# Optimization experiments

Measured on AMD Instinct MI355X. Metric: run time of the kernel, lower is better.

The kernel has to match this reference:

```python
import jax, jax.numpy as jnp
import numpy as np

D_MODEL, N_HEADS, D_K, BASE, EPS = 1024, 16, 64, 10000, 1e-6
SCALE = 1.0 / np.sqrt(D_K)


def rope(x):
    # x: [b, s, h, d]
    b, s, h, d = x.shape
    d2 = d // 2
    theta = 1.0 / (BASE ** (jnp.arange(0, d, 2, dtype=jnp.float32) / d))  # [d2]
    idx_theta = jnp.arange(s, dtype=jnp.float32)[:, None] * theta[None, :]  # [s, d2]
    idx_theta2 = jnp.concatenate([idx_theta, idx_theta], axis=1)  # [s, d]
    cos = jnp.cos(idx_theta2)[None, :, None, :]
    sin = jnp.sin(idx_theta2)[None, :, None, :]
    neg_half = jnp.concatenate([-x[..., d2:], x[..., :d2]], axis=-1)
    return x * cos + neg_half * sin


def setup_inputs() -> dict:
    key = jax.random.key(0)
    ks = jax.random.split(key, 10)
    B, S = 2, 2048
    std = 1.0 / np.sqrt(D_MODEL)
    return {
        "h": jax.random.normal(ks[0], (B, S, D_MODEL), dtype=jnp.float32),
        "wq": jax.random.normal(ks[1], (D_MODEL, N_HEADS * D_K), dtype=jnp.float32) * std,
        "bq": jnp.zeros((N_HEADS * D_K,), dtype=jnp.float32),
        "wk": jax.random.normal(ks[2], (D_MODEL, N_HEADS * D_K), dtype=jnp.float32) * std,
        "bk": jnp.zeros((N_HEADS * D_K,), dtype=jnp.float32),
        "wv": jax.random.normal(ks[3], (D_MODEL, N_HEADS * D_K), dtype=jnp.float32) * std,
        "bv": jnp.zeros((N_HEADS * D_K,), dtype=jnp.float32),
        "wo": jax.random.normal(ks[4], (N_HEADS * D_K, D_MODEL), dtype=jnp.float32) * std,
        "bo": jnp.zeros((D_MODEL,), dtype=jnp.float32),
        "g": jnp.ones((D_MODEL,), dtype=jnp.float32),
    }


def reference(h, wq, bq, wk, bk, wv, bv, wo, bo, g):
    B, S, _ = h.shape
    h_res = h
    # RMSNorm
    hn = h * jax.lax.rsqrt(jnp.mean(h * h, axis=-1, keepdims=True) + EPS) * g
    mh = (B, S, N_HEADS, D_K)
    q = (hn @ wq + bq).reshape(mh)
    k = (hn @ wk + bk).reshape(mh)
    v = (hn @ wv + bv).reshape(mh)
    q, k = rope(q), rope(k)
    attn = jnp.einsum('bihd,bjhd->bhij', q, k) * SCALE
    mask = jnp.tril(jnp.ones((S, S), dtype=bool))
    attn = jnp.where(mask, attn, -jnp.inf)
    attn = jax.nn.softmax(attn, axis=-1)
    out = jnp.einsum('bhij,bjhd->bihd', attn, v).reshape(B, S, N_HEADS * D_K)
    return out @ wo + bo + h_res
```

## Files before the change

### kernel.cpp

```cpp
#include <hip/hip_runtime.h>
#include <hip/hip_bf16.h>

#define D_MODEL 1024
#define NH 16
#define DK 64
#define SEQ 2048
#define BATCH 2
#define NTOK (BATCH * SEQ)
#define EPS 1e-6f

typedef __attribute__((ext_vector_type(4))) float f32x4;
typedef __attribute__((ext_vector_type(16))) float f32x16;
typedef __attribute__((ext_vector_type(8))) short s16x8;
typedef unsigned int u32;
typedef __hip_bfloat16 bf16;

#define AS1 __attribute__((address_space(1)))
#define AS3 __attribute__((address_space(3)))

static __device__ __forceinline__ s16x8 ld8(const bf16* p) {
    return *reinterpret_cast<const s16x8*>(p);
}
static __device__ __forceinline__ float b2f(short s) {
    return __uint_as_float(((u32)(unsigned short)s) << 16);
}

static __device__ __forceinline__ u32 cvtpk(float lo, float hi) {
    u32 r;
    asm volatile("v_cvt_pk_bf16_f32 %0, %1, %2" : "=v"(r) : "v"(lo), "v"(hi));
    return r;
}
static __device__ __forceinline__ void swap32(u32& a, u32& b) {
    asm volatile("v_permlane32_swap_b32 %0, %1" : "+v"(a), "+v"(b));
}
static __device__ __forceinline__ float exp2f_fast(float x) {
    float r;
    asm("v_exp_f32 %0, %1" : "=v"(r) : "v"(x));
    return r;
}
static __device__ __forceinline__ void gld_lds16(const bf16* g, bf16* l) {
    __builtin_amdgcn_global_load_lds((const AS1 void*)g, (AS3 void*)l, 16, 0, 0);
}

union W4 { s16x8 v; u32 w[4]; };

#define LDSW(arr, row, kc) ld8(&arr[(row)][(((kc) ^ ((row) & 7)) << 3)])

__global__ __launch_bounds__(256) void k_prep(const float* __restrict__ h,
                                              const float* __restrict__ g,
                                              const float* __restrict__ wq,
                                              const float* __restrict__ wk,
                                              const float* __restrict__ wv,
                                              const float* __restrict__ wo,
                                              bf16* __restrict__ hn,
                                              bf16* __restrict__ wallT,
                                              float2* __restrict__ tab) {
    const int bid = blockIdx.x;
    const int tid = threadIdx.x;
    if (bid < 4096) {
        const int row = bid;
        const float4 x = reinterpret_cast<const float4*>(h + (size_t)row * D_MODEL)[tid];
        float ss = x.x * x.x + x.y * x.y + x.z * x.z + x.w * x.w;
#pragma unroll
        for (int off = 32; off; off >>= 1) ss += __shfl_xor(ss, off);
        __shared__ float red[4];
        if ((tid & 63) == 0) red[tid >> 6] = ss;
        __syncthreads();
        const float tot = red[0] + red[1] + red[2] + red[3];
        const float rs = rsqrtf(tot * (1.0f / D_MODEL) + EPS);
        const float4 gg = reinterpret_cast<const float4*>(g)[tid];
        bf16* o = hn + (size_t)row * D_MODEL + tid * 4;
        o[0] = __float2bfloat16(x.x * rs * gg.x);
        o[1] = __float2bfloat16(x.y * rs * gg.y);
        o[2] = __float2bfloat16(x.z * rs * gg.z);
        o[3] = __float2bfloat16(x.w * rs * gg.w);
        if (row < 256) {
            const int idx = row * 256 + tid;
            const int s = idx >> 5, i = idx & 31;
            const float theta = __expf(-(float)i * 0.28782313662425572f);
            float sn, cs;
            sincosf((float)s * theta, &sn, &cs);
            tab[idx] = make_float2(cs, sn);
        }
    } else {
        __shared__ float t[32][33];
        const int bid2 = bid - 4096;
        const int kt = (bid2 & 31) * 32;
        const int by = bid2 >> 5;
        const int nt = by * 32;
        const float* W = (by < 32) ? wq : (by < 64) ? wk : (by < 96) ? wv : wo;
        const int nl = nt & (D_MODEL - 1);
        const int tx = tid & 31, ty = tid >> 5;
#pragma unroll
        for (int i = 0; i < 4; i++)
            t[ty + 8 * i][tx] = W[(size_t)(kt + ty + 8 * i) * D_MODEL + nl + tx];
        __syncthreads();
#pragma unroll
        for (int i = 0; i < 4; i++)
            wallT[(size_t)(nt + ty + 8 * i) * D_MODEL + kt + tx] = __float2bfloat16(t[tx][ty + 8 * i]);
    }
}

__global__ __launch_bounds__(256) void k_gemm64_qkv(const bf16* __restrict__ A,
                                                    const bf16* __restrict__ Bt,
                                                    const float* __restrict__ bq,
                                                    const float* __restrict__ bk,
                                                    const float* __restrict__ bv,
                                                    const float2* __restrict__ tab,
                                                    bf16* __restrict__ qb,
                                                    bf16* __restrict__ kpk,
                                                    bf16* __restrict__ vpk) {
    __shared__ __align__(16) char smem[16384];
    bf16(*As)[64] = (bf16(*)[64])smem;
    bf16(*Bs)[64] = (bf16(*)[64])(smem + 8192);
    const int tid = threadIdx.x;
    const int w = tid >> 6, lane = tid & 63, l16 = lane & 15, lq = lane >> 4;
    const int wr = w >> 1, wc = w & 1;
    const int col0 = blockIdx.x * 64;
    const int row0 = blockIdx.y * 64;
    const int grow = lane >> 3;
    const int scol = (((lane & 7) ^ grow) << 3);
    f32x4 acc[2][2];
#pragma unroll
    for (int i = 0; i < 2; i++)
#pragma unroll
        for (int j = 0; j < 2; j++) acc[i][j] = f32x4{0, 0, 0, 0};

    for (int kt = 0; kt < D_MODEL; kt += 64) {
        gld_lds16(A + (size_t)(row0 + w * 16 + grow) * D_MODEL + kt + scol,      &As[w * 16][0]);
        gld_lds16(A + (size_t)(row0 + w * 16 + 8 + grow) * D_MODEL + kt + scol,  &As[w * 16 + 8][0]);
        gld_lds16(Bt + (size_t)(col0 + w * 16 + grow) * D_MODEL + kt + scol,     &Bs[w * 16][0]);
        gld_lds16(Bt + (size_t)(col0 + w * 16 + 8 + grow) * D_MODEL + kt + scol, &Bs[w * 16 + 8][0]);
        __syncthreads();
        s16x8 af[2][2], bfr[2][2];
#pragma unroll
        for (int mi = 0; mi < 2; mi++)
#pragma unroll
            for (int ks = 0; ks < 2; ks++)
                af[mi][ks] = LDSW(As, wr * 32 + mi * 16 + l16, ks * 4 + lq);
#pragma unroll
        for (int ni = 0; ni < 2; ni++)
#pragma unroll
            for (int ks = 0; ks < 2; ks++)
                bfr[ni][ks] = LDSW(Bs, wc * 32 + ni * 16 + l16, ks * 4 + lq);
        __builtin_amdgcn_s_setprio(1);
#pragma unroll
        for (int ks = 0; ks < 2; ks++)
#pragma unroll
            for (int mi = 0; mi < 2; mi++)
#pragma unroll
                for (int ni = 0; ni < 2; ni++)
                    acc[mi][ni] = __builtin_amdgcn_mfma_f32_16x16x32_bf16(af[mi][ks], bfr[ni][ks], acc[mi][ni], 0, 0, 0);
        __builtin_amdgcn_s_setprio(0);
        __syncthreads();
    }

    const int sect = col0 >> 10;
    const int b_ = row0 >> 11;
    const int head = (col0 & 1023) >> 6;
    if (sect == 2) {
        const int e0 = (lq & 1) * 4;
        const int tileL = (row0 & (SEQ - 1)) >> 6;
        bf16* dstH = vpk + ((size_t)(b_ * NH + head) << 17);
#pragma unroll
        for (int ni = 0; ni < 2; ni++) {
            const int dloc = wc * 32 + ni * 16 + l16;
            const float bs = bv[(col0 & 1023) + dloc];
#pragma unroll
            for (int mi = 0; mi < 2; mi++) {
                const int m = wr * 2 + mi;
                size_t off = ((((size_t)(tileL * 2 + (dloc >> 5)) * 4 + m) * 64
                               + ((lq >> 1) & 1) * 32 + (dloc & 31)) << 3) + e0;
                uint2 pv;
                pv.x = cvtpk(acc[mi][ni][0] + bs, acc[mi][ni][1] + bs);
                pv.y = cvtpk(acc[mi][ni][2] + bs, acc[mi][ni][3] + bs);
                *reinterpret_cast<uint2*>(dstH + off) = pv;
            }
        }
        return;
    }
    bf16(*Cs)[72] = (bf16(*)[72])smem;
    const float* bias = (sect == 0) ? bq : bk;
#pragma unroll
    for (int ni = 0; ni < 2; ni++) {
        const int cl = wc * 32 + ni * 16 + l16;
        const float bs = bias[(col0 & 1023) + cl];
#pragma unroll
        for (int mi = 0; mi < 2; mi++) {
            const int rl = wr * 32 + mi * 16 + lq * 4;
#pragma unroll
            for (int r = 0; r < 4; r++)
                Cs[rl + r][cl] = __float2bfloat16(acc[mi][ni][r] + bs);
        }
    }
    __syncthreads();
    const int row = tid >> 2, q = tid & 3;
    const int s_ = (row0 + row) & (SEQ - 1);
    const float2* tb = tab + s_ * 32 + q * 8;
    const float qs = (sect == 0) ? 0.18033688011112042f : 1.0f;
    const s16x8 vlo = ld8(&Cs[row][q * 8]);
    const s16x8 vhi = ld8(&Cs[row][q * 8 + 32]);
    u32 plo[4], phi[4];
#pragma unroll
    for (int e2 = 0; e2 < 4; e2++) {
        float a[2], b[2];
#pragma unroll
        for (int k = 0; k < 2; k++) {
            const int e = e2 * 2 + k;
            const float2 cs = tb[e];
            const float x1 = b2f(vlo[e]), x2 = b2f(vhi[e]);
            a[k] = (x1 * cs.x - x2 * cs.y) * qs;
            b[k] = (x2 * cs.x + x1 * cs.y) * qs;
        }
        plo[e2] = cvtpk(a[0], a[1]);
        phi[e2] = cvtpk(b[0], b[1]);
    }
    if (sect == 0) {
        bf16* qdst = qb + (((size_t)(b_ * NH + head) * SEQ + s_) << 6);
        *reinterpret_cast<uint4*>(qdst + q * 8)      = make_uint4(plo[0], plo[1], plo[2], plo[3]);
        *reinterpret_cast<uint4*>(qdst + 32 + q * 8) = make_uint4(phi[0], phi[1], phi[2], phi[3]);
    } else {
        bf16* kdst = kpk + ((size_t)(b_ * NH + head) << 17);
        const int jb = s_ >> 5, j31 = s_ & 31;
        const size_t offL = (((size_t)(jb * 4 + (q >> 1)) * 64 + (q & 1) * 32 + j31) << 3);
        const size_t offH = (((size_t)(jb * 4 + ((q + 4) >> 1)) * 64 + ((q + 4) & 1) * 32 + j31) << 3);
        *reinterpret_cast<uint4*>(kdst + offL) = make_uint4(plo[0], plo[1], plo[2], plo[3]);
        *reinterpret_cast<uint4*>(kdst + offH) = make_uint4(phi[0], phi[1], phi[2], phi[3]);
    }
}

__global__ __launch_bounds__(256) void k_attn9(const bf16* __restrict__ qg,
                                               const bf16* __restrict__ kp,
                                               const bf16* __restrict__ vp,
                                               bf16* __restrict__ ao) {
    const int tid = threadIdx.x;
    const int w = tid >> 6;
    const int lane = tid & 63;
    const int l31 = lane & 31;
    const int hi = lane >> 5;
    const int bid = blockIdx.x;
    const int blk = (bid >> 3) & 15;
    const int bh  = (bid & 7) + ((bid >> 7) << 3);
    int pos;
    switch (w) {
        case 0:  pos = blk;      break;
        case 1:  pos = 31 - blk; break;
        case 2:  pos = 32 + blk; break;
        default: pos = 63 - blk; break;
    }
    const int qw = pos << 5;
    const int qrow = qw + l31;

    const bf16* qptr = qg + (((size_t)bh * SEQ + qrow) << 6) + 8 * hi;
    s16x8 qf[4];
#pragma unroll
    for (int t = 0; t < 4; t++) qf[t] = ld8(qptr + 16 * t);

    f32x16 o0, o1;
#pragma unroll
    for (int r = 0; r < 16; r++) { o0[r] = 0.0f; o1[r] = 0.0f; }
    float l4[4] = {0.0f, 0.0f, 0.0f, 0.0f};

    const int nfull = qw >> 6;
    const int ntot  = (qw + 95) >> 6;
    const bf16* kbase = kp + ((size_t)bh << 17);
    const bf16* vbase = vp + ((size_t)bh << 17);

    s16x8 kA[8], kB[8], vC[8];
#pragma unroll
    for (int t = 0; t < 8; t++) kA[t] = ld8(kbase + (((size_t)t * 64 + lane) << 3));

    auto att_step = [&](s16x8(&KC)[8], s16x8(&KN)[8], const int kt) {
        const int kb = kt << 6;
#pragma unroll
        for (int t = 0; t < 8; t++)
            vC[t] = ld8(vbase + (((size_t)(kt * 8 + t) * 64 + lane) << 3));
        f32x16 s0, s1;
#pragma unroll
        for (int r = 0; r < 16; r++) { s0[r] = 0.0f; s1[r] = 0.0f; }
        __builtin_amdgcn_s_setprio(1);
#pragma unroll
        for (int t = 0; t < 4; t++) {
            s0 = __builtin_amdgcn_mfma_f32_32x32x16_bf16(KC[t],     qf[t], s0, 0, 0, 0);
            s1 = __builtin_amdgcn_mfma_f32_32x32x16_bf16(KC[4 + t], qf[t], s1, 0, 0, 0);
        }
        __builtin_amdgcn_s_setprio(0);
        const int ktn = (kt + 1 < ntot) ? kt + 1 : kt;
#pragma unroll
        for (int t = 0; t < 8; t++)
            KN[t] = ld8(kbase + (((size_t)(ktn * 8 + t) * 64 + lane) << 3));
        float p[32];
#pragma unroll
        for (int r = 0; r < 16; r++) { p[r] = s0[r]; p[16 + r] = s1[r]; }
        if (kt >= nfull) {
#pragma unroll
            for (int r = 0; r < 32; r++) {
                const int j = kb + 8 * (r >> 2) + (r & 3) + 4 * hi;
                if (j > qrow) p[r] = -3.0e38f;
            }
        }
#pragma unroll
        for (int r = 0; r < 32; r++) { p[r] = exp2f_fast(p[r]); l4[r & 3] += p[r]; }
        u32 pk_[16];
#pragma unroll
        for (int a = 0; a < 8; a++) {
            pk_[2 * a]     = cvtpk(p[4 * a],     p[4 * a + 1]);
            pk_[2 * a + 1] = cvtpk(p[4 * a + 2], p[4 * a + 3]);
        }
        __builtin_amdgcn_s_setprio(1);
#pragma unroll
        for (int m = 0; m < 4; m++) {
            u32 b0 = pk_[4 * m],     b2 = pk_[4 * m + 2];
            u32 b1 = pk_[4 * m + 1], b3 = pk_[4 * m + 3];
            swap32(b0, b2);
            swap32(b1, b3);
            W4 B; B.w[0] = b0; B.w[1] = b1; B.w[2] = b2; B.w[3] = b3;
            o0 = __builtin_amdgcn_mfma_f32_32x32x16_bf16(vC[m],     B.v, o0, 0, 0, 0);
            o1 = __builtin_amdgcn_mfma_f32_32x32x16_bf16(vC[4 + m], B.v, o1, 0, 0, 0);
        }
        __builtin_amdgcn_s_setprio(0);
    };

    int kt = 0;
    for (;;) {
        att_step(kA, kB, kt); if (++kt == ntot) break;
        att_step(kB, kA, kt); if (++kt == ntot) break;
    }

    float rs = (l4[0] + l4[1]) + (l4[2] + l4[3]);
    rs += __shfl_xor(rs, 32);
    const float inv = 1.0f / rs;
    const int b_ = bh >> 4, h_ = bh & (NH - 1);
    bf16* orow = ao + (((size_t)(b_ * SEQ + qrow)) << 10) + (h_ << 6);
#pragma unroll
    for (int g = 0; g < 4; g++) {
        {
            uint2 val;
            val.x = cvtpk(o0[4 * g] * inv, o0[4 * g + 1] * inv);
            val.y = cvtpk(o0[4 * g + 2] * inv, o0[4 * g + 3] * inv);
            *reinterpret_cast<uint2*>(orow + 8 * g + 4 * hi) = val;
        }
        {
            uint2 val;
            val.x = cvtpk(o1[4 * g] * inv, o1[4 * g + 1] * inv);
            val.y = cvtpk(o1[4 * g + 2] * inv, o1[4 * g + 3] * inv);
            *reinterpret_cast<uint2*>(orow + 32 + 8 * g + 4 * hi) = val;
        }
    }
}

__global__ __launch_bounds__(256) void k_gemm64_out(const bf16* __restrict__ A,
                                                    const bf16* __restrict__ Bt,
                                                    const float* __restrict__ bo,
                                                    const float* __restrict__ hres,
                                                    float* __restrict__ out) {
    __shared__ __align__(16) char smem[16384];
    bf16(*As)[64] = (bf16(*)[64])smem;
    bf16(*Bs)[64] = (bf16(*)[64])(smem + 8192);
    const int tid = threadIdx.x;
    const int w = tid >> 6, lane = tid & 63, l16 = lane & 15, lq = lane >> 4;
    const int wr = w >> 1, wc = w & 1;
    const int col0 = blockIdx.x * 64;
    const int row0 = blockIdx.y * 64;
    const int grow = lane >> 3;
    const int scol = (((lane & 7) ^ grow) << 3);
    f32x4 acc[2][2];
#pragma unroll
    for (int i = 0; i < 2; i++)
#pragma unroll
        for (int j = 0; j < 2; j++) acc[i][j] = f32x4{0, 0, 0, 0};

    for (int kt = 0; kt < D_MODEL; kt += 64) {
        gld_lds16(A + (size_t)(row0 + w * 16 + grow) * D_MODEL + kt + scol,      &As[w * 16][0]);
        gld_lds16(A + (size_t)(row0 + w * 16 + 8 + grow) * D_MODEL + kt + scol,  &As[w * 16 + 8][0]);
        gld_lds16(Bt + (size_t)(col0 + w * 16 + grow) * D_MODEL + kt + scol,     &Bs[w * 16][0]);
        gld_lds16(Bt + (size_t)(col0 + w * 16 + 8 + grow) * D_MODEL + kt + scol, &Bs[w * 16 + 8][0]);
        __syncthreads();
        s16x8 af[2][2], bfr[2][2];
#pragma unroll
        for (int mi = 0; mi < 2; mi++)
#pragma unroll
            for (int ks = 0; ks < 2; ks++)
                af[mi][ks] = LDSW(As, wr * 32 + mi * 16 + l16, ks * 4 + lq);
#pragma unroll
        for (int ni = 0; ni < 2; ni++)
#pragma unroll
            for (int ks = 0; ks < 2; ks++)
                bfr[ni][ks] = LDSW(Bs, wc * 32 + ni * 16 + l16, ks * 4 + lq);
        __builtin_amdgcn_s_setprio(1);
#pragma unroll
        for (int ks = 0; ks < 2; ks++)
#pragma unroll
            for (int mi = 0; mi < 2; mi++)
#pragma unroll
                for (int ni = 0; ni < 2; ni++)
                    acc[mi][ni] = __builtin_amdgcn_mfma_f32_16x16x32_bf16(af[mi][ks], bfr[ni][ks], acc[mi][ni], 0, 0, 0);
        __builtin_amdgcn_s_setprio(0);
        __syncthreads();
    }
#pragma unroll
    for (int ni = 0; ni < 2; ni++) {
        const int col = col0 + wc * 32 + ni * 16 + l16;
        const float bs = bo[col];
#pragma unroll
        for (int mi = 0; mi < 2; mi++) {
#pragma unroll
            for (int r = 0; r < 4; r++) {
                const int row = row0 + wr * 32 + mi * 16 + lq * 4 + r;
                out[(size_t)row * D_MODEL + col] =
                    acc[mi][ni][r] + bs + hres[(size_t)row * D_MODEL + col];
            }
        }
    }
}

extern "C" void kernel_launch(void* const* d_in, const int* in_sizes, int n_in,
                              void* d_out, int out_size, void* d_ws, size_t ws_size,
                              hipStream_t stream) {
    (void)in_sizes; (void)n_in; (void)out_size; (void)ws_size;
    const float* h  = (const float*)d_in[0];
    const float* wq = (const float*)d_in[1];
    const float* bq = (const float*)d_in[2];
    const float* wk = (const float*)d_in[3];
    const float* bk = (const float*)d_in[4];
    const float* wv = (const float*)d_in[5];
    const float* bv = (const float*)d_in[6];
    const float* wo = (const float*)d_in[7];
    const float* bo = (const float*)d_in[8];
    const float* g  = (const float*)d_in[9];
    float* out = (float*)d_out;

    char* ws = (char*)d_ws;
    size_t off = 0;
    auto carve = [&](size_t bytes) {
        void* p = ws + off;
        off += (bytes + 255) & ~(size_t)255;
        return p;
    };
    bf16* hn    = (bf16*)carve((size_t)NTOK * D_MODEL * 2);
    bf16* wallT = (bf16*)carve((size_t)4 * D_MODEL * D_MODEL * 2);
    bf16* wqkvT = wallT;
    bf16* woT   = wallT + (size_t)3 * D_MODEL * D_MODEL;
    bf16* qb    = (bf16*)carve((size_t)BATCH * NH * SEQ * DK * 2);
    bf16* kpk   = (bf16*)carve((size_t)BATCH * NH * SEQ * DK * 2);
    bf16* vpk   = (bf16*)carve((size_t)BATCH * NH * SEQ * DK * 2);
    bf16* ao    = (bf16*)carve((size_t)NTOK * D_MODEL * 2);
    float2* tab = (float2*)carve((size_t)SEQ * 32 * sizeof(float2));

    k_prep<<<8192, 256, 0, stream>>>(h, g, wq, wk, wv, wo, hn, wallT, tab);
    k_gemm64_qkv<<<dim3(48, 64), 256, 0, stream>>>(hn, wqkvT, bq, bk, bv, tab, qb, kpk, vpk);
    k_attn9<<<512, 256, 0, stream>>>(qb, kpk, vpk, ao);
    k_gemm64_out<<<dim3(16, 64), 256, 0, stream>>>(ao, woT, bo, h, out);
}
```

Before: 107.2 us.

## Compute Q, K and V for one head per block to reuse A tiles

The QKV projection kernel now assigns one head per block and computes all three Q/K/V sections, loading the activation tile once and reusing it against three weight tiles. The grid shrinks threefold and each block does three times the MFMA work per barrier. The RoPE epilogue loops over Q and K through shared memory. This trades fewer blocks, higher register use and larger LDS for reduced activation traffic.

```diff
diff --git a/kernel.cpp b/kernel.cpp
--- a/kernel.cpp
+++ b/kernel.cpp
@@ -101,131 +101,142 @@
     }
 }
 
-__global__ __launch_bounds__(256) void k_gemm64_qkv(const bf16* __restrict__ A,
-                                                    const bf16* __restrict__ Bt,
-                                                    const float* __restrict__ bq,
-                                                    const float* __restrict__ bk,
-                                                    const float* __restrict__ bv,
-                                                    const float2* __restrict__ tab,
-                                                    bf16* __restrict__ qb,
-                                                    bf16* __restrict__ kpk,
-                                                    bf16* __restrict__ vpk) {
-    __shared__ __align__(16) char smem[16384];
+__global__ __launch_bounds__(256) void k_gemm64_qkv3(const bf16* __restrict__ A,
+                                                     const bf16* __restrict__ Bt,
+                                                     const float* __restrict__ bq,
+                                                     const float* __restrict__ bk,
+                                                     const float* __restrict__ bv,
+                                                     const float2* __restrict__ tab,
+                                                     bf16* __restrict__ qb,
+                                                     bf16* __restrict__ kpk,
+                                                     bf16* __restrict__ vpk) {
+    __shared__ __align__(16) char smem[32768];
     bf16(*As)[64] = (bf16(*)[64])smem;
     bf16(*Bs)[64] = (bf16(*)[64])(smem + 8192);
     const int tid = threadIdx.x;
     const int w = tid >> 6, lane = tid & 63, l16 = lane & 15, lq = lane >> 4;
     const int wr = w >> 1, wc = w & 1;
-    const int col0 = blockIdx.x * 64;
+    const int head = blockIdx.x;
     const int row0 = blockIdx.y * 64;
     const int grow = lane >> 3;
     const int scol = (((lane & 7) ^ grow) << 3);
-    f32x4 acc[2][2];
-#pragma unroll
-    for (int i = 0; i < 2; i++)
-#pragma unroll
-        for (int j = 0; j < 2; j++) acc[i][j] = f32x4{0, 0, 0, 0};
+    f32x4 acc[3][2][2];
+#pragma unroll
+    for (int s = 0; s < 3; s++)
+#pragma unroll
+        for (int i = 0; i < 2; i++)
+#pragma unroll
+            for (int j = 0; j < 2; j++) acc[s][i][j] = f32x4{0, 0, 0, 0};
 
     for (int kt = 0; kt < D_MODEL; kt += 64) {
-        gld_lds16(A + (size_t)(row0 + w * 16 + grow) * D_MODEL + kt + scol,      &As[w * 16][0]);
-        gld_lds16(A + (size_t)(row0 + w * 16 + 8 + grow) * D_MODEL + kt + scol,  &As[w * 16 + 8][0]);
-        gld_lds16(Bt + (size_t)(col0 + w * 16 + grow) * D_MODEL + kt + scol,     &Bs[w * 16][0]);
-        gld_lds16(Bt + (size_t)(col0 + w * 16 + 8 + grow) * D_MODEL + kt + scol, &Bs[w * 16 + 8][0]);
-        __syncthreads();
-        s16x8 af[2][2], bfr[2][2];
+        gld_lds16(A + (size_t)(row0 + w * 16 + grow) * D_MODEL + kt + scol,     &As[w * 16][0]);
+        gld_lds16(A + (size_t)(row0 + w * 16 + 8 + grow) * D_MODEL + kt + scol, &As[w * 16 + 8][0]);
+#pragma unroll
+        for (int s = 0; s < 3; s++) {
+            const size_t brow = (size_t)(s * 1024 + head * 64);
+            gld_lds16(Bt + (brow + w * 16 + grow) * D_MODEL + kt + scol,     &Bs[s * 64 + w * 16][0]);
+            gld_lds16(Bt + (brow + w * 16 + 8 + grow) * D_MODEL + kt + scol, &Bs[s * 64 + w * 16 + 8][0]);
+        }
+        __syncthreads();
+        s16x8 af[2][2];
 #pragma unroll
         for (int mi = 0; mi < 2; mi++)
 #pragma unroll
             for (int ks = 0; ks < 2; ks++)
                 af[mi][ks] = LDSW(As, wr * 32 + mi * 16 + l16, ks * 4 + lq);
-#pragma unroll
-        for (int ni = 0; ni < 2; ni++)
+        __builtin_amdgcn_s_setprio(1);
+#pragma unroll
+        for (int s = 0; s < 3; s++) {
+            s16x8 bfr[2][2];
+#pragma unroll
+            for (int ni = 0; ni < 2; ni++)
+#pragma unroll
+                for (int ks = 0; ks < 2; ks++)
+                    bfr[ni][ks] = LDSW(Bs, s * 64 + wc * 32 + ni * 16 + l16, ks * 4 + lq);
 #pragma unroll
             for (int ks = 0; ks < 2; ks++)
-                bfr[ni][ks] = LDSW(Bs, wc * 32 + ni * 16 + l16, ks * 4 + lq);
-        __builtin_amdgcn_s_setprio(1);
-#pragma unroll
-        for (int ks = 0; ks < 2; ks++)
-#pragma unroll
-            for (int mi = 0; mi < 2; mi++)
-#pragma unroll
-                for (int ni = 0; ni < 2; ni++)
-                    acc[mi][ni] = __builtin_amdgcn_mfma_f32_16x16x32_bf16(af[mi][ks], bfr[ni][ks], acc[mi][ni], 0, 0, 0);
+#pragma unroll
+                for (int mi = 0; mi < 2; mi++)
+#pragma unroll
+                    for (int ni = 0; ni < 2; ni++)
+                        acc[s][mi][ni] = __builtin_amdgcn_mfma_f32_16x16x32_bf16(af[mi][ks], bfr[ni][ks], acc[s][mi][ni], 0, 0, 0);
+        }
         __builtin_amdgcn_s_setprio(0);
         __syncthreads();
     }
 
-    const int sect = col0 >> 10;
     const int b_ = row0 >> 11;
-    const int head = (col0 & 1023) >> 6;
-    if (sect == 2) {
+    {
         const int e0 = (lq & 1) * 4;
         const int tileL = (row0 & (SEQ - 1)) >> 6;
         bf16* dstH = vpk + ((size_t)(b_ * NH + head) << 17);
 #pragma unroll
         for (int ni = 0; ni < 2; ni++) {
             const int dloc = wc * 32 + ni * 16 + l16;
-            const float bs = bv[(col0 & 1023) + dloc];
+            const float bs = bv[head * 64 + dloc];
 #pragma unroll
             for (int mi = 0; mi < 2; mi++) {
                 const int m = wr * 2 + mi;
                 size_t off = ((((size_t)(tileL * 2 + (dloc >> 5)) * 4 + m) * 64
                                + ((lq >> 1) & 1) * 32 + (dloc & 31)) << 3) + e0;
                 uint2 pv;
-                pv.x = cvtpk(acc[mi][ni][0] + bs, acc[mi][ni][1] + bs);
-                pv.y = cvtpk(acc[mi][ni][2] + bs, acc[mi][ni][3] + bs);
+                pv.x = cvtpk(acc[2][mi][ni][0] + bs, acc[2][mi][ni][1] + bs);
+                pv.y = cvtpk(acc[2][mi][ni][2] + bs, acc[2][mi][ni][3] + bs);
                 *reinterpret_cast<uint2*>(dstH + off) = pv;
             }
         }
-        return;
     }
     bf16(*Cs)[72] = (bf16(*)[72])smem;
-    const float* bias = (sect == 0) ? bq : bk;
-#pragma unroll
-    for (int ni = 0; ni < 2; ni++) {
-        const int cl = wc * 32 + ni * 16 + l16;
-        const float bs = bias[(col0 & 1023) + cl];
-#pragma unroll
-        for (int mi = 0; mi < 2; mi++) {
-            const int rl = wr * 32 + mi * 16 + lq * 4;
-#pragma unroll
-            for (int r = 0; r < 4; r++)
-                Cs[rl + r][cl] = __float2bfloat16(acc[mi][ni][r] + bs);
-        }
-    }
-    __syncthreads();
     const int row = tid >> 2, q = tid & 3;
     const int s_ = (row0 + row) & (SEQ - 1);
     const float2* tb = tab + s_ * 32 + q * 8;
-    const float qs = (sect == 0) ? 0.18033688011112042f : 1.0f;
-    const s16x8 vlo = ld8(&Cs[row][q * 8]);
-    const s16x8 vhi = ld8(&Cs[row][q * 8 + 32]);
-    u32 plo[4], phi[4];
-#pragma unroll
-    for (int e2 = 0; e2 < 4; e2++) {
-        float a[2], b[2];
-#pragma unroll
-        for (int k = 0; k < 2; k++) {
-            const int e = e2 * 2 + k;
-            const float2 cs = tb[e];
-            const float x1 = b2f(vlo[e]), x2 = b2f(vhi[e]);
-            a[k] = (x1 * cs.x - x2 * cs.y) * qs;
-            b[k] = (x2 * cs.x + x1 * cs.y) * qs;
-        }
-        plo[e2] = cvtpk(a[0], a[1]);
-        phi[e2] = cvtpk(b[0], b[1]);
-    }
-    if (sect == 0) {
-        bf16* qdst = qb + (((size_t)(b_ * NH + head) * SEQ + s_) << 6);
-        *reinterpret_cast<uint4*>(qdst + q * 8)      = make_uint4(plo[0], plo[1], plo[2], plo[3]);
-        *reinterpret_cast<uint4*>(qdst + 32 + q * 8) = make_uint4(phi[0], phi[1], phi[2], phi[3]);
-    } else {
-        bf16* kdst = kpk + ((size_t)(b_ * NH + head) << 17);
-        const int jb = s_ >> 5, j31 = s_ & 31;
-        const size_t offL = (((size_t)(jb * 4 + (q >> 1)) * 64 + (q & 1) * 32 + j31) << 3);
-        const size_t offH = (((size_t)(jb * 4 + ((q + 4) >> 1)) * 64 + ((q + 4) & 1) * 32 + j31) << 3);
-        *reinterpret_cast<uint4*>(kdst + offL) = make_uint4(plo[0], plo[1], plo[2], plo[3]);
-        *reinterpret_cast<uint4*>(kdst + offH) = make_uint4(phi[0], phi[1], phi[2], phi[3]);
+#pragma unroll
+    for (int sec = 0; sec < 2; sec++) {
+        const float* bias = sec ? bk : bq;
+        __syncthreads();
+#pragma unroll
+        for (int ni = 0; ni < 2; ni++) {
+            const int cl = wc * 32 + ni * 16 + l16;
+            const float bs = bias[head * 64 + cl];
+#pragma unroll
+            for (int mi = 0; mi < 2; mi++) {
+                const int rl = wr * 32 + mi * 16 + lq * 4;
+#pragma unroll
+                for (int r = 0; r < 4; r++)
+                    Cs[rl + r][cl] = __float2bfloat16(acc[sec][mi][ni][r] + bs);
+            }
+        }
+        __syncthreads();
+        const float qs = sec ? 1.0f : 0.18033688011112042f;
+        const s16x8 vlo = ld8(&Cs[row][q * 8]);
+        const s16x8 vhi = ld8(&Cs[row][q * 8 + 32]);
+        u32 plo[4], phi[4];
+#pragma unroll
+        for (int e2 = 0; e2 < 4; e2++) {
+            float a[2], b[2];
+#pragma unroll
+            for (int k = 0; k < 2; k++) {
+                const int e = e2 * 2 + k;
+                const float2 cs = tb[e];
+                const float x1 = b2f(vlo[e]), x2 = b2f(vhi[e]);
+                a[k] = (x1 * cs.x - x2 * cs.y) * qs;
+                b[k] = (x2 * cs.x + x1 * cs.y) * qs;
+            }
+            plo[e2] = cvtpk(a[0], a[1]);
+            phi[e2] = cvtpk(b[0], b[1]);
+        }
+        if (sec == 0) {
+            bf16* qdst = qb + (((size_t)(b_ * NH + head) * SEQ + s_) << 6);
+            *reinterpret_cast<uint4*>(qdst + q * 8)      = make_uint4(plo[0], plo[1], plo[2], plo[3]);
+            *reinterpret_cast<uint4*>(qdst + 32 + q * 8) = make_uint4(phi[0], phi[1], phi[2], phi[3]);
+        } else {
+            bf16* kdst = kpk + ((size_t)(b_ * NH + head) << 17);
+            const int jb = s_ >> 5, j31 = s_ & 31;
+            const size_t offL = (((size_t)(jb * 4 + (q >> 1)) * 64 + (q & 1) * 32 + j31) << 3);
+            const size_t offH = (((size_t)(jb * 4 + ((q + 4) >> 1)) * 64 + ((q + 4) & 1) * 32 + j31) << 3);
+            *reinterpret_cast<uint4*>(kdst + offL) = make_uint4(plo[0], plo[1], plo[2], plo[3]);
+            *reinterpret_cast<uint4*>(kdst + offH) = make_uint4(phi[0], phi[1], phi[2], phi[3]);
+        }
     }
 }
 
@@ -448,7 +459,7 @@
     float2* tab = (float2*)carve((size_t)SEQ * 32 * sizeof(float2));
 
     k_prep<<<8192, 256, 0, stream>>>(h, g, wq, wk, wv, wo, hn, wallT, tab);
-    k_gemm64_qkv<<<dim3(48, 64), 256, 0, stream>>>(hn, wqkvT, bq, bk, bv, tab, qb, kpk, vpk);
+    k_gemm64_qkv3<<<dim3(16, 64), 256, 0, stream>>>(hn, wqkvT, bq, bk, bv, tab, qb, kpk, vpk);
     k_attn9<<<512, 256, 0, stream>>>(qb, kpk, vpk, ao);
     k_gemm64_out<<<dim3(16, 64), 256, 0, stream>>>(ao, woT, bo, h, out);
 }
```

Result: no change. 107.6 us (+0.4%).
